# Performance work log

Hardware: AMD Instinct MI355X
Metric: run time of the kernel (lower is better)

The kernel has to match this reference:

```python
import jax, jax.numpy as jnp
import numpy as np

N, E, B = 50000, 400000, 128
F_IN, EDIM, EMB, H = 64, 8, 64, 4
HC = EMB * H  # 256
L = 3          # gnn_layers
DN = 256       # dense_neurons
NEG_SLOPE = 0.2
EPS = 1e-5


def setup_inputs():
    key = jax.random.key(0)
    ks = jax.random.split(key, 32)
    s = 0.05
    d = {}
    d["x"] = jax.random.normal(ks[0], (N, F_IN), jnp.float32)
    d["edge_index"] = jax.random.randint(ks[1], (2, E), 0, N, jnp.int32)
    d["edge_attr"] = jax.random.normal(ks[2], (E, EDIM), jnp.float32)
    d["mol_formal_charge"] = jax.random.normal(ks[3], (B,), jnp.float32)
    d["mol_nrot"] = jax.random.normal(ks[4], (B,), jnp.float32)
    d["batch_index"] = jnp.sort(jax.random.randint(ks[5], (N,), 0, B, jnp.int32))
    # GATv2 params, stacked over L layers (in_dim == EMB == F_IN for all layers)
    d["gat_Wl"] = jax.random.normal(ks[6], (L, F_IN, HC), jnp.float32) * s
    d["gat_Wr"] = jax.random.normal(ks[7], (L, F_IN, HC), jnp.float32) * s
    d["gat_We"] = jax.random.normal(ks[8], (L, EDIM, HC), jnp.float32) * s
    d["gat_att"] = jax.random.normal(ks[9], (L, H, EMB), jnp.float32) * s
    d["gat_b"] = jnp.zeros((L, HC), jnp.float32)
    d["tr_W"] = jax.random.normal(ks[10], (L, HC, EMB), jnp.float32) * s
    d["tr_b"] = jnp.zeros((L, EMB), jnp.float32)
    d["bn_g"] = jnp.ones((L, EMB), jnp.float32)
    d["bn_b"] = jnp.zeros((L, EMB), jnp.float32)
    d["gate_W"] = jax.random.normal(ks[11], (EMB, 1), jnp.float32) * s
    d["gate_b"] = jnp.zeros((1,), jnp.float32)
    d["lin1_W"] = jax.random.normal(ks[12], (EMB + 2, DN), jnp.float32) * s
    d["lin1_b"] = jnp.zeros((DN,), jnp.float32)
    d["fc1_W"] = jax.random.normal(ks[13], (DN, DN // 2), jnp.float32) * s
    d["fc1_b"] = jnp.zeros((DN // 2,), jnp.float32)
    d["fc2_W"] = jax.random.normal(ks[14], (DN // 2, DN // 4), jnp.float32) * s
    d["fc2_b"] = jnp.zeros((DN // 4,), jnp.float32)
    d["out_W"] = jax.random.normal(ks[15], (DN // 4, 1), jnp.float32) * s
    d["out_b"] = jnp.zeros((1,), jnp.float32)
    return d


def _seg_softmax(logits, seg, num):
    # numerically stable per-segment softmax over leading axis
    mx = jax.ops.segment_max(logits, seg, num_segments=num)
    ex = jnp.exp(logits - mx[seg])
    den = jax.ops.segment_sum(ex, seg, num_segments=num)
    return ex / den[seg]


def reference(x, edge_index, edge_attr, mol_formal_charge, mol_nrot, batch_index,
              gat_Wl, gat_Wr, gat_We, gat_att, gat_b, tr_W, tr_b, bn_g, bn_b,
              gate_W, gate_b, lin1_W, lin1_b, fc1_W, fc1_b, fc2_W, fc2_b,
              out_W, out_b):
    src, dst = edge_index[0], edge_index[1]  # messages flow src -> dst
    h = x
    for l in range(L):
        xl = (h @ gat_Wl[l]).reshape(N, H, EMB)
        xr = (h @ gat_Wr[l]).reshape(N, H, EMB)
        ea = (edge_attr @ gat_We[l]).reshape(E, H, EMB)
        xls = xl[src]                                   # [E,H,C]
        m = jax.nn.leaky_relu(xls + xr[dst] + ea, NEG_SLOPE)
        logit = jnp.einsum('ehc,hc->eh', m, gat_att[l])  # [E,H]
        alpha = _seg_softmax(logit, dst, N)              # [E,H]
        agg = jax.ops.segment_sum(alpha[:, :, None] * xls, dst, num_segments=N)
        h = agg.reshape(N, HC) + gat_b[l]
        h = jax.nn.relu(h @ tr_W[l] + tr_b[l])
        # BatchNorm1d (training-mode batch stats, biased var)
        mu = h.mean(0)
        var = h.var(0)
        h = (h - mu) / jnp.sqrt(var + EPS) * bn_g[l] + bn_b[l]
    # AttentionalAggregation pooling
    gate = h @ gate_W + gate_b                           # [N,1]
    w = _seg_softmax(gate, batch_index, B)
    pooled = jax.ops.segment_sum(w * h, batch_index, num_segments=B)  # [B,EMB]
    z = jnp.concatenate([pooled, mol_formal_charge[:, None], mol_nrot[:, None]], axis=1)
    z = jax.nn.relu(z @ lin1_W + lin1_b)
    z = jax.nn.relu(z @ fc1_W + fc1_b)
    z = jax.nn.relu(z @ fc2_W + fc2_b)
    return z @ out_W + out_b                             # [B,1]
```

## Files before the change

### kernel.cpp

```cpp
#include <hip/hip_runtime.h>

#define NN 50000
#define NE 400000
#define NB 128
#define NINF (-__builtin_inff())

__global__ __launch_bounds__(256) void k_hist(const int* __restrict__ dstv, int* __restrict__ deg) {
    int e = blockIdx.x * 256 + threadIdx.x;
    if (e < NE) atomicAdd(&deg[dstv[e]], 1);
}

__global__ __launch_bounds__(1024) void k_scan(const int* __restrict__ deg, int* __restrict__ rowptr) {
    __shared__ int wsum[16];
    __shared__ int total_s;
    const int tid = threadIdx.x, lane = tid & 63, w = tid >> 6;
    if (tid == 0) rowptr[0] = 0;
    int carry = 0;
    for (int base = 0; base < NN; base += 1024) {
        int i = base + tid;
        int v = (i < NN) ? deg[i] : 0;
        int incl = v;
        #pragma unroll
        for (int off = 1; off < 64; off <<= 1) {
            int t = __shfl_up(incl, off);
            if (lane >= off) incl += t;
        }
        if (lane == 63) wsum[w] = incl;
        __syncthreads();
        if (tid < 16) {
            int s = wsum[tid];
            int si = s;
            #pragma unroll
            for (int off = 1; off < 16; off <<= 1) {
                int t = __shfl_up(si, off, 16);
                if (tid >= off) si += t;
            }
            wsum[tid] = si - s;
            if (tid == 15) total_s = si;
        }
        __syncthreads();
        if (i < NN) rowptr[i + 1] = carry + wsum[w] + incl;
        carry += total_s;
        __syncthreads();
    }
}

__global__ __launch_bounds__(256) void k_scatter(const int* __restrict__ dstv, const int* __restrict__ rowptr,
                                                 int* __restrict__ cnt, int* __restrict__ eid) {
    int e = blockIdx.x * 256 + threadIdx.x;
    if (e < NE) {
        int d = dstv[e];
        int pos = rowptr[d] + atomicAdd(&cnt[d], 1);
        eid[pos] = e;
    }
}

__global__ __launch_bounds__(256) void k_permute(const int* __restrict__ eid, const int* __restrict__ srcv,
                                                 const float* __restrict__ eattr, int* __restrict__ src_perm,
                                                 float4* __restrict__ ea_perm) {
    int p = blockIdx.x * 256 + threadIdx.x;
    if (p < NE) {
        int e = eid[p];
        src_perm[p] = srcv[e];
        ea_perm[p * 2] = ((const float4*)eattr)[e * 2];
        ea_perm[p * 2 + 1] = ((const float4*)eattr)[e * 2 + 1];
    }
}

__global__ __launch_bounds__(256) void k_gemm64(const float* __restrict__ A, const float* __restrict__ Wl,
                                                const float* __restrict__ Wr, float* __restrict__ Cl,
                                                float* __restrict__ Cr, const float* __restrict__ bnp) {
    __shared__ float As[64 * 64];
    __shared__ float Ws[64 * 128];
    const int tid = threadIdx.x;
    const int mat = blockIdx.y >> 1, ch = blockIdx.y & 1;
    const float* W = mat ? Wr : Wl;
    float* C = mat ? Cr : Cl;
    const int r0b = blockIdx.x * 64;

    for (int i = tid; i < 2048; i += 256) {
        const int k = i >> 5, c4 = i & 31;
        float4 v = ((const float4*)W)[k * 64 + ch * 32 + c4];
        if (bnp) {
            const float s = bnp[128 + k];
            v.x *= s; v.y *= s; v.z *= s; v.w *= s;
        }
        ((float4*)Ws)[i] = v;
    }
    for (int i = tid; i < 1024; i += 256) {
        const int r = i >> 4, c4 = i & 15;
        const int rg = (r0b + r < NN) ? (r0b + r) : (NN - 1);
        ((float4*)As)[i] = ((const float4*)A)[rg * 16 + c4];
    }
    __syncthreads();

    const int cg = tid & 31;
    const int rq = tid >> 5;
    float acc[8][4];
    if (bnp) {
        const float* shW = bnp + 256 + mat * 256 + ch * 128 + cg * 4;
        #pragma unroll
        for (int rr = 0; rr < 8; ++rr) {
            acc[rr][0] = shW[0]; acc[rr][1] = shW[1]; acc[rr][2] = shW[2]; acc[rr][3] = shW[3];
        }
    } else {
        #pragma unroll
        for (int rr = 0; rr < 8; ++rr)
            acc[rr][0] = acc[rr][1] = acc[rr][2] = acc[rr][3] = 0.f;
    }

    for (int kq = 0; kq < 16; ++kq) {
        float4 av[8];
        #pragma unroll
        for (int rr = 0; rr < 8; ++rr)
            av[rr] = ((const float4*)As)[(rq * 8 + rr) * 16 + kq];
        #pragma unroll
        for (int kk = 0; kk < 4; ++kk) {
            const float4 w = *(const float4*)(Ws + ((kq * 4 + kk) << 7) + (cg << 2));
            #pragma unroll
            for (int rr = 0; rr < 8; ++rr) {
                const float a = reinterpret_cast<const float*>(&av[rr])[kk];
                acc[rr][0] = fmaf(a, w.x, acc[rr][0]);
                acc[rr][1] = fmaf(a, w.y, acc[rr][1]);
                acc[rr][2] = fmaf(a, w.z, acc[rr][2]);
                acc[rr][3] = fmaf(a, w.w, acc[rr][3]);
            }
        }
    }
    #pragma unroll
    for (int rr = 0; rr < 8; ++rr) {
        const int r = r0b + rq * 8 + rr;
        if (r < NN)
            *(float4*)(C + (size_t)r * 256 + ch * 128 + cg * 4) =
                make_float4(acc[rr][0], acc[rr][1], acc[rr][2], acc[rr][3]);
    }
}

template <bool PERM>
__global__ __launch_bounds__(256, 4) void k_agg(const float* __restrict__ xl, float* __restrict__ xragg,
                                                const float* __restrict__ att, const float* __restrict__ gatb,
                                                const int* __restrict__ rowptr, const int* __restrict__ eid,
                                                const int* __restrict__ srcv, const float* __restrict__ eattr,
                                                const int* __restrict__ src_perm, const float4* __restrict__ ea_perm,
                                                const float* __restrict__ We) {
    const int lane = threadIdx.x & 63;
    const float4 we0 = ((const float4*)(We + 0 * 256))[lane];
    const float4 we1 = ((const float4*)(We + 1 * 256))[lane];
    const float4 we2 = ((const float4*)(We + 2 * 256))[lane];
    const float4 we3 = ((const float4*)(We + 3 * 256))[lane];
    const float4 we4 = ((const float4*)(We + 4 * 256))[lane];
    const float4 we5 = ((const float4*)(We + 5 * 256))[lane];
    const float4 we6 = ((const float4*)(We + 6 * 256))[lane];
    const float4 we7 = ((const float4*)(We + 7 * 256))[lane];
    const float4 attf = ((const float4*)att)[lane];
    const float4 gbf = ((const float4*)gatb)[lane];
    const int nw = gridDim.x * (blockDim.x >> 6);
    int wid = blockIdx.x * (blockDim.x >> 6) + (threadIdx.x >> 6);

#define LOADE(X, idx)                                                          \
    {                                                                          \
        int s_;                                                                \
        const float4* eap_;                                                    \
        if (PERM) {                                                            \
            s_ = src_perm[idx];                                                \
            eap_ = ea_perm + (size_t)(idx) * 2;                                \
        } else {                                                               \
            const int e_ = eid[idx];                                           \
            s_ = srcv[e_];                                                     \
            eap_ = (const float4*)(eattr + (size_t)e_ * 8);                    \
        }                                                                      \
        X##x = ((const float4*)(xl + (size_t)s_ * 256))[lane];                 \
        X##a = eap_[0];                                                        \
        X##b = eap_[1];                                                        \
    }

#define PROC(X, M, D, C0, C1, C2, C3)                                          \
    {                                                                          \
        float v0 = fmaf(X##a.x, we0.x, xr.x), v1 = fmaf(X##a.x, we0.y, xr.y);  \
        float v2 = fmaf(X##a.x, we0.z, xr.z), v3 = fmaf(X##a.x, we0.w, xr.w);  \
        v0 = fmaf(X##a.y, we1.x, v0); v1 = fmaf(X##a.y, we1.y, v1);            \
        v2 = fmaf(X##a.y, we1.z, v2); v3 = fmaf(X##a.y, we1.w, v3);            \
        v0 = fmaf(X##a.z, we2.x, v0); v1 = fmaf(X##a.z, we2.y, v1);            \
        v2 = fmaf(X##a.z, we2.z, v2); v3 = fmaf(X##a.z, we2.w, v3);            \
        v0 = fmaf(X##a.w, we3.x, v0); v1 = fmaf(X##a.w, we3.y, v1);            \
        v2 = fmaf(X##a.w, we3.z, v2); v3 = fmaf(X##a.w, we3.w, v3);            \
        v0 = fmaf(X##b.x, we4.x, v0); v1 = fmaf(X##b.x, we4.y, v1);            \
        v2 = fmaf(X##b.x, we4.z, v2); v3 = fmaf(X##b.x, we4.w, v3);            \
        v0 = fmaf(X##b.y, we5.x, v0); v1 = fmaf(X##b.y, we5.y, v1);            \
        v2 = fmaf(X##b.y, we5.z, v2); v3 = fmaf(X##b.y, we5.w, v3);            \
        v0 = fmaf(X##b.z, we6.x, v0); v1 = fmaf(X##b.z, we6.y, v1);            \
        v2 = fmaf(X##b.z, we6.z, v2); v3 = fmaf(X##b.z, we6.w, v3);            \
        v0 = fmaf(X##b.w, we7.x, v0); v1 = fmaf(X##b.w, we7.y, v1);            \
        v2 = fmaf(X##b.w, we7.z, v2); v3 = fmaf(X##b.w, we7.w, v3);            \
        v0 += X##x.x; v1 += X##x.y; v2 += X##x.z; v3 += X##x.w;                \
        v0 = fmaxf(v0, 0.2f * v0); v1 = fmaxf(v1, 0.2f * v1);                  \
        v2 = fmaxf(v2, 0.2f * v2); v3 = fmaxf(v3, 0.2f * v3);                  \
        float part = v0 * attf.x;                                              \
        part = fmaf(v1, attf.y, part);                                         \
        part = fmaf(v2, attf.z, part);                                         \
        part = fmaf(v3, attf.w, part);                                         \
        part += __shfl_xor(part, 1);                                           \
        part += __shfl_xor(part, 2);                                           \
        part += __shfl_xor(part, 4);                                           \
        part += __shfl_xor(part, 8);                                           \
        const float mn = fmaxf(M, part);                                       \
        const float scl = __expf(M - mn);                                      \
        const float p = __expf(part - mn);                                     \
        D = fmaf(D, scl, p);                                                   \
        C0 = fmaf(C0, scl, p * X##x.x);                                        \
        C1 = fmaf(C1, scl, p * X##x.y);                                        \
        C2 = fmaf(C2, scl, p * X##x.z);                                        \
        C3 = fmaf(C3, scl, p * X##x.w);                                        \
        M = mn;                                                                \
    }

    for (int n = wid; n < NN; n += nw) {
        const int e0 = rowptr[n], e1 = rowptr[n + 1];
        const float4 xr = ((const float4*)(xragg + (size_t)n * 256))[lane];
        float mA = NINF, dA = 0.f, cA0 = 0.f, cA1 = 0.f, cA2 = 0.f, cA3 = 0.f;
        float mB = NINF, dB = 0.f, cB0 = 0.f, cB1 = 0.f, cB2 = 0.f, cB3 = 0.f;
        float4 Ax, Aa, Ab, Bx, Ba, Bb;
        if (e0 < e1) LOADE(A, e0);
        if (e0 + 1 < e1) LOADE(B, e0 + 1);
        int i = e0;
        for (; i + 5 < e1; i += 4) {
            float4 Cx, Ca, Cb, Dx, Da, Db;
            LOADE(C, i + 2);
            LOADE(D, i + 3);
            PROC(A, mA, dA, cA0, cA1, cA2, cA3);
            PROC(B, mB, dB, cB0, cB1, cB2, cB3);
            LOADE(A, i + 4);
            LOADE(B, i + 5);
            PROC(C, mA, dA, cA0, cA1, cA2, cA3);
            PROC(D, mB, dB, cB0, cB1, cB2, cB3);
        }
        if (i < e1) PROC(A, mA, dA, cA0, cA1, cA2, cA3);
        if (i + 1 < e1) PROC(B, mB, dB, cB0, cB1, cB2, cB3);
        for (int j = i + 2; j < e1; ++j) {
            LOADE(A, j);
            PROC(A, mA, dA, cA0, cA1, cA2, cA3);
        }
        float4 o;
        if (e1 > e0) {
            const float m = fmaxf(mA, mB);
            const float wA = __expf(mA - m), wB = __expf(mB - m);
            const float inv = 1.0f / fmaf(wA, dA, wB * dB);
            o.x = fmaf((wA * cA0 + wB * cB0), inv, gbf.x);
            o.y = fmaf((wA * cA1 + wB * cB1), inv, gbf.y);
            o.z = fmaf((wA * cA2 + wB * cB2), inv, gbf.z);
            o.w = fmaf((wA * cA3 + wB * cB3), inv, gbf.w);
        } else {
            o = gbf;
        }
        ((float4*)(xragg + (size_t)n * 256))[lane] = o;
    }
#undef LOADE
#undef PROC
}

__global__ __launch_bounds__(256) void k_tr(const float* __restrict__ A, const float* __restrict__ W,
                                            const float* __restrict__ bias, float* __restrict__ Hout,
                                            float* __restrict__ stats) {
    __shared__ float As[64 * 68];
    __shared__ float Ws[64 * 64];
    __shared__ float red[128];
    const int tid = threadIdx.x;
    const int cg = tid & 15;
    const int rq = tid >> 4;
    const int r0b = blockIdx.x * 64;

    float acc[4][4];
    {
        const float b0 = bias[cg * 4], b1 = bias[cg * 4 + 1], b2 = bias[cg * 4 + 2], b3 = bias[cg * 4 + 3];
        #pragma unroll
        for (int rr = 0; rr < 4; ++rr) { acc[rr][0] = b0; acc[rr][1] = b1; acc[rr][2] = b2; acc[rr][3] = b3; }
    }

    for (int kc = 0; kc < 4; ++kc) {
        if (kc) __syncthreads();
        for (int i = tid; i < 1024; i += 256)
            ((float4*)Ws)[i] = ((const float4*)(W + kc * 4096))[i];
        for (int i = tid; i < 1024; i += 256) {
            const int r = i >> 4, c4 = i & 15;
            const int rg = (r0b + r < NN) ? (r0b + r) : (NN - 1);
            *(float4*)(As + r * 68 + c4 * 4) = ((const float4*)A)[(size_t)rg * 64 + kc * 16 + c4];
        }
        __syncthreads();
        for (int kq = 0; kq < 16; ++kq) {
            float4 av[4];
            #pragma unroll
            for (int rr = 0; rr < 4; ++rr)
                av[rr] = *(const float4*)(As + (rq * 4 + rr) * 68 + kq * 4);
            #pragma unroll
            for (int kk = 0; kk < 4; ++kk) {
                const float4 w = *(const float4*)(Ws + ((kq * 4 + kk) << 6) + (cg << 2));
                #pragma unroll
                for (int rr = 0; rr < 4; ++rr) {
                    const float a = reinterpret_cast<const float*>(&av[rr])[kk];
                    acc[rr][0] = fmaf(a, w.x, acc[rr][0]);
                    acc[rr][1] = fmaf(a, w.y, acc[rr][1]);
                    acc[rr][2] = fmaf(a, w.z, acc[rr][2]);
                    acc[rr][3] = fmaf(a, w.w, acc[rr][3]);
                }
            }
        }
    }
    float lsum[4] = {0.f, 0.f, 0.f, 0.f}, lsq[4] = {0.f, 0.f, 0.f, 0.f};
    #pragma unroll
    for (int rr = 0; rr < 4; ++rr) {
        const int r = r0b + rq * 4 + rr;
        if (r < NN) {
            float v0 = fmaxf(acc[rr][0], 0.f), v1 = fmaxf(acc[rr][1], 0.f);
            float v2 = fmaxf(acc[rr][2], 0.f), v3 = fmaxf(acc[rr][3], 0.f);
            lsum[0] += v0; lsum[1] += v1; lsum[2] += v2; lsum[3] += v3;
            lsq[0] = fmaf(v0, v0, lsq[0]); lsq[1] = fmaf(v1, v1, lsq[1]);
            lsq[2] = fmaf(v2, v2, lsq[2]); lsq[3] = fmaf(v3, v3, lsq[3]);
            *(float4*)(Hout + (size_t)r * 64 + cg * 4) = make_float4(v0, v1, v2, v3);
        }
    }
    __syncthreads();
    if (tid < 128) red[tid] = 0.f;
    __syncthreads();
    #pragma unroll
    for (int j = 0; j < 4; ++j) {
        atomicAdd(&red[cg * 4 + j], lsum[j]);
        atomicAdd(&red[64 + cg * 4 + j], lsq[j]);
    }
    __syncthreads();
    if (tid < 64) {
        atomicAdd(&stats[tid], red[tid]);
        atomicAdd(&stats[64 + tid], red[64 + tid]);
    }
}

__global__ __launch_bounds__(256) void k_bn_finalize(float* __restrict__ st, const float* __restrict__ g,
                                                     const float* __restrict__ b, const float* __restrict__ Wln,
                                                     const float* __restrict__ Wrn) {
    __shared__ float sh_s[64];
    const int tid = threadIdx.x;
    if (tid < 64) {
        const float mu = st[tid] * (1.0f / (float)NN);
        const float var = st[64 + tid] * (1.0f / (float)NN) - mu * mu;
        const float rstd = rsqrtf(var + 1e-5f);
        const float sc = g[tid] * rstd;
        const float sh = fmaf(-mu, sc, b[tid]);
        st[128 + tid] = sc;
        st[192 + tid] = sh;
        sh_s[tid] = sh;
    }
    __syncthreads();
    if (Wln) {
        float al = 0.f, ar = 0.f;
        for (int k = 0; k < 64; ++k) {
            al = fmaf(sh_s[k], Wln[k * 256 + tid], al);
            ar = fmaf(sh_s[k], Wrn[k * 256 + tid], ar);
        }
        st[256 + tid] = al;
        st[512 + tid] = ar;
    }
}

__global__ __launch_bounds__(256) void k_pool(const float* __restrict__ h, const float* __restrict__ gw,
                                              const int* __restrict__ bidx, const float* __restrict__ st,
                                              float* __restrict__ pooled) {
    __shared__ float gate_s[1024];
    __shared__ float red[4];
    __shared__ float pp[4][64];
    const int b = blockIdx.x, tid = threadIdx.x, lane = tid & 63, w = tid >> 6;
    int lo = 0, hi = NN;
    while (lo < hi) { int mid = (lo + hi) >> 1; if (bidx[mid] < b) lo = mid + 1; else hi = mid; }
    const int s0 = lo;
    lo = 0; hi = NN;
    while (lo < hi) { int mid = (lo + hi) >> 1; if (bidx[mid] < b + 1) lo = mid + 1; else hi = mid; }
    const int s1 = lo;
    const int seg = s1 - s0;
    if (seg == 0) {
        if (tid < 64) pooled[b * 64 + tid] = st[192 + tid];
        return;
    }
    const float gwv = gw[lane] * st[128 + lane];
    for (int i = s0 + w; i < s1; i += 4) {
        float p = h[(size_t)i * 64 + lane] * gwv;
        #pragma unroll
        for (int off = 32; off; off >>= 1) p += __shfl_xor(p, off);
        if (lane == 0) gate_s[i - s0] = p;
    }
    __syncthreads();
    float v = NINF;
    for (int i = tid; i < seg; i += 256) v = fmaxf(v, gate_s[i]);
    #pragma unroll
    for (int off = 32; off; off >>= 1) v = fmaxf(v, __shfl_xor(v, off));
    if (lane == 0) red[w] = v;
    __syncthreads();
    const float mx = fmaxf(fmaxf(red[0], red[1]), fmaxf(red[2], red[3]));
    __syncthreads();
    float d = 0.f;
    for (int i = tid; i < seg; i += 256) {
        const float ex = __expf(gate_s[i] - mx);
        gate_s[i] = ex;
        d += ex;
    }
    #pragma unroll
    for (int off = 32; off; off >>= 1) d += __shfl_xor(d, off);
    if (lane == 0) red[w] = d;
    __syncthreads();
    const float den = red[0] + red[1] + red[2] + red[3];
    const int c = tid & 63, ro = tid >> 6;
    float acc = 0.f;
    for (int i = s0 + ro; i < s1; i += 4) acc = fmaf(gate_s[i - s0], h[(size_t)i * 64 + c], acc);
    pp[ro][c] = acc;
    __syncthreads();
    if (ro == 0) {
        const float raw = (pp[0][c] + pp[1][c] + pp[2][c] + pp[3][c]) / den;
        pooled[b * 64 + c] = fmaf(raw, st[128 + c], st[192 + c]);
    }
}

__global__ __launch_bounds__(256) void k_head(const float* __restrict__ pooled, const float* __restrict__ fc,
                                              const float* __restrict__ nrot, const float* __restrict__ W1,
                                              const float* __restrict__ b1, const float* __restrict__ W2,
                                              const float* __restrict__ b2, const float* __restrict__ W3,
                                              const float* __restrict__ b3, const float* __restrict__ W4,
                                              const float* __restrict__ b4, float* __restrict__ out) {
    __shared__ float z[66], a1[256], a2[128], a3[64];
    const int b = blockIdx.x, tid = threadIdx.x;
    if (tid < 64) z[tid] = pooled[b * 64 + tid];
    if (tid == 64) z[64] = fc[b];
    if (tid == 65) z[65] = nrot[b];
    __syncthreads();
    float s = b1[tid];
    for (int k = 0; k < 66; ++k) s = fmaf(z[k], W1[k * 256 + tid], s);
    a1[tid] = fmaxf(s, 0.f);
    __syncthreads();
    if (tid < 128) {
        float s2 = b2[tid];
        for (int k = 0; k < 256; ++k) s2 = fmaf(a1[k], W2[k * 128 + tid], s2);
        a2[tid] = fmaxf(s2, 0.f);
    }
    __syncthreads();
    if (tid < 64) {
        float s3 = b3[tid];
        for (int k = 0; k < 128; ++k) s3 = fmaf(a2[k], W3[k * 64 + tid], s3);
        a3[tid] = fmaxf(s3, 0.f);
    }
    __syncthreads();
    if (tid < 64) {
        float p = a3[tid] * W4[tid];
        #pragma unroll
        for (int off = 32; off; off >>= 1) p += __shfl_xor(p, off);
        if (tid == 0) out[b] = p + b4[0];
    }
}

extern "C" void kernel_launch(void* const* d_in, const int* in_sizes, int n_in,
                              void* d_out, int out_size, void* d_ws, size_t ws_size,
                              hipStream_t stream) {
    const float* x     = (const float*)d_in[0];
    const int*   ei    = (const int*)d_in[1];
    const float* eattr = (const float*)d_in[2];
    const float* fcv   = (const float*)d_in[3];
    const float* nrot  = (const float*)d_in[4];
    const int*   bidx  = (const int*)d_in[5];
    const float* Wl    = (const float*)d_in[6];
    const float* Wr    = (const float*)d_in[7];
    const float* We    = (const float*)d_in[8];
    const float* att   = (const float*)d_in[9];
    const float* gatb  = (const float*)d_in[10];
    const float* trW   = (const float*)d_in[11];
    const float* trb   = (const float*)d_in[12];
    const float* bng   = (const float*)d_in[13];
    const float* bnb   = (const float*)d_in[14];
    const float* gateW = (const float*)d_in[15];
    const float* W1    = (const float*)d_in[17];
    const float* b1    = (const float*)d_in[18];
    const float* W2    = (const float*)d_in[19];
    const float* b2    = (const float*)d_in[20];
    const float* W3    = (const float*)d_in[21];
    const float* b3    = (const float*)d_in[22];
    const float* W4    = (const float*)d_in[23];
    const float* b4    = (const float*)d_in[24];
    float* out = (float*)d_out;

    const int* srcv = ei;
    const int* dstv = ei + NE;

    char* w = (char*)d_ws;
    float*  xl       = (float*)(w);
    float*  xragg    = (float*)(w + 51200000);
    float*  hbuf     = (float*)(w + 102400000);
    int*    deg      = (int*)  (w + 102400000);
    int*    cnt      = (int*)  (w + 102600000);
    int*    eid      = (int*)  (w + 115200000);
    int*    rowptr   = (int*)  (w + 116800000);
    float*  stats    = (float*)(w + 117000064);
    float*  pooled   = (float*)(w + 117009280);
    int*    src_perm = (int*)  (w + 117042048);
    float4* ea_perm  = (float4*)(w + 118642048);
    const bool use_perm = (ws_size >= (size_t)131442048);

    hipMemsetAsync(deg, 0, 400000, stream);
    hipMemsetAsync(stats, 0, 9216, stream);
    k_hist<<<(NE + 255) / 256, 256, 0, stream>>>(dstv, deg);
    k_scan<<<1, 1024, 0, stream>>>(deg, rowptr);
    k_scatter<<<(NE + 255) / 256, 256, 0, stream>>>(dstv, rowptr, cnt, eid);
    if (use_perm)
        k_permute<<<(NE + 255) / 256, 256, 0, stream>>>(eid, srcv, eattr, src_perm, ea_perm);

    const float* hin = x;
    for (int l = 0; l < 3; ++l) {
        const float* bnp = (l == 0) ? nullptr : (stats + (l - 1) * 768);
        dim3 gg((NN + 63) / 64, 4);
        k_gemm64<<<gg, 256, 0, stream>>>(hin, Wl + l * 16384, Wr + l * 16384, xl, xragg, bnp);
        if (use_perm)
            k_agg<true><<<2048, 256, 0, stream>>>(xl, xragg, att + l * 256, gatb + l * 256, rowptr,
                                                  eid, srcv, eattr, src_perm, ea_perm, We + l * 2048);
        else
            k_agg<false><<<2048, 256, 0, stream>>>(xl, xragg, att + l * 256, gatb + l * 256, rowptr,
                                                   eid, srcv, eattr, src_perm, ea_perm, We + l * 2048);
        k_tr<<<(NN + 63) / 64, 256, 0, stream>>>(xragg, trW + l * 16384, trb + l * 64, hbuf, stats + l * 768);
        k_bn_finalize<<<1, 256, 0, stream>>>(stats + l * 768, bng + l * 64, bnb + l * 64,
                                             (l < 2) ? (Wl + (l + 1) * 16384) : nullptr,
                                             (l < 2) ? (Wr + (l + 1) * 16384) : nullptr);
        hin = hbuf;
    }
    k_pool<<<NB, 256, 0, stream>>>(hbuf, gateW, bidx, stats + 2 * 768, pooled);
    k_head<<<NB, 256, 0, stream>>>(pooled, fcv, nrot, W1, b1, W2, b2, W3, b3, W4, b4, out);
}
```

Measured before the change: 792.3 us.

## Drop online-max softmax, fuse permute into scatter and BN finalize into consumers

Replaces the two-stream online-softmax aggregation with a single accumulator that exponentiates logits directly without max subtraction, using DPP adds for the 16-lane reduction and a lighter 2-deep prefetch. Fuses the edge permutation into the scatter kernel, folds the batch-norm finalize into the next GEMM and the pooling kernel, and merges pooling with the MLP head. This removes exp work and several kernel launches. It risks overflow for large attention logits and recomputes the shift-weight product in every GEMM block.

```diff
diff --git a/kernel.cpp b/kernel.cpp
--- a/kernel.cpp
+++ b/kernel.cpp
@@ -4,6 +4,18 @@
 #define NE 400000
 #define NB 128
 #define NINF (-__builtin_inff())
+
+__device__ __forceinline__ float dpp_add16(float x) {
+    int v = __float_as_int(x);
+    x += __int_as_float(__builtin_amdgcn_update_dpp(0, v, 0xB1, 0xF, 0xF, true));
+    v = __float_as_int(x);
+    x += __int_as_float(__builtin_amdgcn_update_dpp(0, v, 0x4E, 0xF, 0xF, true));
+    v = __float_as_int(x);
+    x += __int_as_float(__builtin_amdgcn_update_dpp(0, v, 0x141, 0xF, 0xF, true));
+    v = __float_as_int(x);
+    x += __int_as_float(__builtin_amdgcn_update_dpp(0, v, 0x140, 0xF, 0xF, true));
+    return x;
+}
 
 __global__ __launch_bounds__(256) void k_hist(const int* __restrict__ dstv, int* __restrict__ deg) {
     int e = blockIdx.x * 256 + threadIdx.x;
@@ -45,44 +57,53 @@
     }
 }
 
-__global__ __launch_bounds__(256) void k_scatter(const int* __restrict__ dstv, const int* __restrict__ rowptr,
-                                                 int* __restrict__ cnt, int* __restrict__ eid) {
+__global__ __launch_bounds__(256) void k_scatter(const int* __restrict__ dstv, const int* __restrict__ srcv,
+                                                 const float* __restrict__ eattr, const int* __restrict__ rowptr,
+                                                 int* __restrict__ cnt, int* __restrict__ eid,
+                                                 int* __restrict__ src_perm, float4* __restrict__ ea_perm,
+                                                 int use_perm) {
     int e = blockIdx.x * 256 + threadIdx.x;
     if (e < NE) {
         int d = dstv[e];
         int pos = rowptr[d] + atomicAdd(&cnt[d], 1);
         eid[pos] = e;
-    }
-}
-
-__global__ __launch_bounds__(256) void k_permute(const int* __restrict__ eid, const int* __restrict__ srcv,
-                                                 const float* __restrict__ eattr, int* __restrict__ src_perm,
-                                                 float4* __restrict__ ea_perm) {
-    int p = blockIdx.x * 256 + threadIdx.x;
-    if (p < NE) {
-        int e = eid[p];
-        src_perm[p] = srcv[e];
-        ea_perm[p * 2] = ((const float4*)eattr)[e * 2];
-        ea_perm[p * 2 + 1] = ((const float4*)eattr)[e * 2 + 1];
+        if (use_perm) {
+            src_perm[pos] = srcv[e];
+            ea_perm[(size_t)pos * 2] = ((const float4*)eattr)[e * 2];
+            ea_perm[(size_t)pos * 2 + 1] = ((const float4*)eattr)[e * 2 + 1];
+        }
     }
 }
 
 __global__ __launch_bounds__(256) void k_gemm64(const float* __restrict__ A, const float* __restrict__ Wl,
                                                 const float* __restrict__ Wr, float* __restrict__ Cl,
-                                                float* __restrict__ Cr, const float* __restrict__ bnp) {
+                                                float* __restrict__ Cr, const float* __restrict__ stats,
+                                                const float* __restrict__ bg, const float* __restrict__ bb) {
     __shared__ float As[64 * 64];
     __shared__ float Ws[64 * 128];
+    __shared__ float sc_s[64], sh_s[64], shW_s[128];
     const int tid = threadIdx.x;
     const int mat = blockIdx.y >> 1, ch = blockIdx.y & 1;
     const float* W = mat ? Wr : Wl;
     float* C = mat ? Cr : Cl;
     const int r0b = blockIdx.x * 64;
 
+    if (stats) {
+        if (tid < 64) {
+            const float mu = stats[tid] * (1.0f / (float)NN);
+            const float var = stats[64 + tid] * (1.0f / (float)NN) - mu * mu;
+            const float rstd = rsqrtf(var + 1e-5f);
+            const float sc = bg[tid] * rstd;
+            sc_s[tid] = sc;
+            sh_s[tid] = fmaf(-mu, sc, bb[tid]);
+        }
+        __syncthreads();
+    }
     for (int i = tid; i < 2048; i += 256) {
         const int k = i >> 5, c4 = i & 31;
         float4 v = ((const float4*)W)[k * 64 + ch * 32 + c4];
-        if (bnp) {
-            const float s = bnp[128 + k];
+        if (stats) {
+            const float s = sc_s[k];
             v.x *= s; v.y *= s; v.z *= s; v.w *= s;
         }
         ((float4*)Ws)[i] = v;
@@ -92,16 +113,22 @@
         const int rg = (r0b + r < NN) ? (r0b + r) : (NN - 1);
         ((float4*)As)[i] = ((const float4*)A)[rg * 16 + c4];
     }
+    if (stats && tid < 128) {
+        const float* wc = W + ch * 128 + tid;
+        float s = 0.f;
+        for (int k = 0; k < 64; ++k) s = fmaf(sh_s[k], wc[k * 256], s);
+        shW_s[tid] = s;
+    }
     __syncthreads();
 
     const int cg = tid & 31;
     const int rq = tid >> 5;
     float acc[8][4];
-    if (bnp) {
-        const float* shW = bnp + 256 + mat * 256 + ch * 128 + cg * 4;
+    if (stats) {
         #pragma unroll
         for (int rr = 0; rr < 8; ++rr) {
-            acc[rr][0] = shW[0]; acc[rr][1] = shW[1]; acc[rr][2] = shW[2]; acc[rr][3] = shW[3];
+            acc[rr][0] = shW_s[cg * 4]; acc[rr][1] = shW_s[cg * 4 + 1];
+            acc[rr][2] = shW_s[cg * 4 + 2]; acc[rr][3] = shW_s[cg * 4 + 3];
         }
     } else {
         #pragma unroll
@@ -174,7 +201,7 @@
         X##b = eap_[1];                                                        \
     }
 
-#define PROC(X, M, D, C0, C1, C2, C3)                                          \
+#define PROC(X)                                                                \
     {                                                                          \
         float v0 = fmaf(X##a.x, we0.x, xr.x), v1 = fmaf(X##a.x, we0.y, xr.y);  \
         float v2 = fmaf(X##a.x, we0.z, xr.z), v3 = fmaf(X##a.x, we0.w, xr.w);  \
@@ -199,56 +226,52 @@
         part = fmaf(v1, attf.y, part);                                         \
         part = fmaf(v2, attf.z, part);                                         \
         part = fmaf(v3, attf.w, part);                                         \
-        part += __shfl_xor(part, 1);                                           \
-        part += __shfl_xor(part, 2);                                           \
-        part += __shfl_xor(part, 4);                                           \
-        part += __shfl_xor(part, 8);                                           \
-        const float mn = fmaxf(M, part);                                       \
-        const float scl = __expf(M - mn);                                      \
-        const float p = __expf(part - mn);                                     \
-        D = fmaf(D, scl, p);                                                   \
-        C0 = fmaf(C0, scl, p * X##x.x);                                        \
-        C1 = fmaf(C1, scl, p * X##x.y);                                        \
-        C2 = fmaf(C2, scl, p * X##x.z);                                        \
-        C3 = fmaf(C3, scl, p * X##x.w);                                        \
-        M = mn;                                                                \
+        part = dpp_add16(part);                                                \
+        const float p = __expf(part);                                          \
+        den += p;                                                              \
+        c0 = fmaf(p, X##x.x, c0);                                              \
+        c1 = fmaf(p, X##x.y, c1);                                              \
+        c2 = fmaf(p, X##x.z, c2);                                              \
+        c3 = fmaf(p, X##x.w, c3);                                              \
     }
 
     for (int n = wid; n < NN; n += nw) {
         const int e0 = rowptr[n], e1 = rowptr[n + 1];
         const float4 xr = ((const float4*)(xragg + (size_t)n * 256))[lane];
-        float mA = NINF, dA = 0.f, cA0 = 0.f, cA1 = 0.f, cA2 = 0.f, cA3 = 0.f;
-        float mB = NINF, dB = 0.f, cB0 = 0.f, cB1 = 0.f, cB2 = 0.f, cB3 = 0.f;
+        float den = 0.f, c0 = 0.f, c1 = 0.f, c2 = 0.f, c3 = 0.f;
         float4 Ax, Aa, Ab, Bx, Ba, Bb;
-        if (e0 < e1) LOADE(A, e0);
-        if (e0 + 1 < e1) LOADE(B, e0 + 1);
-        int i = e0;
-        for (; i + 5 < e1; i += 4) {
-            float4 Cx, Ca, Cb, Dx, Da, Db;
-            LOADE(C, i + 2);
-            LOADE(D, i + 3);
-            PROC(A, mA, dA, cA0, cA1, cA2, cA3);
-            PROC(B, mB, dB, cB0, cB1, cB2, cB3);
-            LOADE(A, i + 4);
-            LOADE(B, i + 5);
-            PROC(C, mA, dA, cA0, cA1, cA2, cA3);
-            PROC(D, mB, dB, cB0, cB1, cB2, cB3);
-        }
-        if (i < e1) PROC(A, mA, dA, cA0, cA1, cA2, cA3);
-        if (i + 1 < e1) PROC(B, mB, dB, cB0, cB1, cB2, cB3);
-        for (int j = i + 2; j < e1; ++j) {
-            LOADE(A, j);
-            PROC(A, mA, dA, cA0, cA1, cA2, cA3);
+        const int cnt = e1 - e0;
+        if (cnt > 0) {
+            LOADE(A, e0);
+            if (cnt > 1) {
+                LOADE(B, e0 + 1);
+                int i = e0;
+                for (; i + 3 < e1; i += 2) {
+                    PROC(A);
+                    LOADE(A, i + 2);
+                    PROC(B);
+                    LOADE(B, i + 3);
+                }
+                const int r = e1 - i;
+                PROC(A);
+                if (r == 3) {
+                    LOADE(A, i + 2);
+                    PROC(B);
+                    PROC(A);
+                } else {
+                    PROC(B);
+                }
+            } else {
+                PROC(A);
+            }
         }
         float4 o;
-        if (e1 > e0) {
-            const float m = fmaxf(mA, mB);
-            const float wA = __expf(mA - m), wB = __expf(mB - m);
-            const float inv = 1.0f / fmaf(wA, dA, wB * dB);
-            o.x = fmaf((wA * cA0 + wB * cB0), inv, gbf.x);
-            o.y = fmaf((wA * cA1 + wB * cB1), inv, gbf.y);
-            o.z = fmaf((wA * cA2 + wB * cB2), inv, gbf.z);
-            o.w = fmaf((wA * cA3 + wB * cB3), inv, gbf.w);
+        if (cnt > 0) {
+            const float inv = 1.0f / den;
+            o.x = fmaf(c0, inv, gbf.x);
+            o.y = fmaf(c1, inv, gbf.y);
+            o.z = fmaf(c2, inv, gbf.z);
+            o.w = fmaf(c3, inv, gbf.w);
         } else {
             o = gbf;
         }
@@ -333,40 +356,29 @@
     }
 }
 
-__global__ __launch_bounds__(256) void k_bn_finalize(float* __restrict__ st, const float* __restrict__ g,
-                                                     const float* __restrict__ b, const float* __restrict__ Wln,
-                                                     const float* __restrict__ Wrn) {
-    __shared__ float sh_s[64];
-    const int tid = threadIdx.x;
-    if (tid < 64) {
-        const float mu = st[tid] * (1.0f / (float)NN);
-        const float var = st[64 + tid] * (1.0f / (float)NN) - mu * mu;
-        const float rstd = rsqrtf(var + 1e-5f);
-        const float sc = g[tid] * rstd;
-        const float sh = fmaf(-mu, sc, b[tid]);
-        st[128 + tid] = sc;
-        st[192 + tid] = sh;
-        sh_s[tid] = sh;
-    }
-    __syncthreads();
-    if (Wln) {
-        float al = 0.f, ar = 0.f;
-        for (int k = 0; k < 64; ++k) {
-            al = fmaf(sh_s[k], Wln[k * 256 + tid], al);
-            ar = fmaf(sh_s[k], Wrn[k * 256 + tid], ar);
-        }
-        st[256 + tid] = al;
-        st[512 + tid] = ar;
-    }
-}
-
-__global__ __launch_bounds__(256) void k_pool(const float* __restrict__ h, const float* __restrict__ gw,
-                                              const int* __restrict__ bidx, const float* __restrict__ st,
-                                              float* __restrict__ pooled) {
+__global__ __launch_bounds__(256) void k_poolhead(const float* __restrict__ h, const float* __restrict__ gw,
+                                                  const int* __restrict__ bidx, const float* __restrict__ stats,
+                                                  const float* __restrict__ bg, const float* __restrict__ bb,
+                                                  const float* __restrict__ fc, const float* __restrict__ nrot,
+                                                  const float* __restrict__ W1, const float* __restrict__ b1,
+                                                  const float* __restrict__ W2, const float* __restrict__ b2,
+                                                  const float* __restrict__ W3, const float* __restrict__ b3,
+                                                  const float* __restrict__ W4, const float* __restrict__ b4,
+                                                  float* __restrict__ out) {
     __shared__ float gate_s[1024];
     __shared__ float red[4];
     __shared__ float pp[4][64];
+    __shared__ float scb[64], shb[64];
+    __shared__ float z[66], a1[256], a2[128], a3[64];
     const int b = blockIdx.x, tid = threadIdx.x, lane = tid & 63, w = tid >> 6;
+    if (tid < 64) {
+        const float mu = stats[tid] * (1.0f / (float)NN);
+        const float var = stats[64 + tid] * (1.0f / (float)NN) - mu * mu;
+        const float rstd = rsqrtf(var + 1e-5f);
+        const float sc = bg[tid] * rstd;
+        scb[tid] = sc;
+        shb[tid] = fmaf(-mu, sc, bb[tid]);
+    }
     int lo = 0, hi = NN;
     while (lo < hi) { int mid = (lo + hi) >> 1; if (bidx[mid] < b) lo = mid + 1; else hi = mid; }
     const int s0 = lo;
@@ -374,11 +386,9 @@
     while (lo < hi) { int mid = (lo + hi) >> 1; if (bidx[mid] < b + 1) lo = mid + 1; else hi = mid; }
     const int s1 = lo;
     const int seg = s1 - s0;
-    if (seg == 0) {
-        if (tid < 64) pooled[b * 64 + tid] = st[192 + tid];
-        return;
-    }
-    const float gwv = gw[lane] * st[128 + lane];
+    __syncthreads();
+
+    const float gwv = gw[lane] * scb[lane];
     for (int i = s0 + w; i < s1; i += 4) {
         float p = h[(size_t)i * 64 + lane] * gwv;
         #pragma unroll
@@ -410,21 +420,10 @@
     for (int i = s0 + ro; i < s1; i += 4) acc = fmaf(gate_s[i - s0], h[(size_t)i * 64 + c], acc);
     pp[ro][c] = acc;
     __syncthreads();
-    if (ro == 0) {
-        const float raw = (pp[0][c] + pp[1][c] + pp[2][c] + pp[3][c]) / den;
-        pooled[b * 64 + c] = fmaf(raw, st[128 + c], st[192 + c]);
-    }
-}
-
-__global__ __launch_bounds__(256) void k_head(const float* __restrict__ pooled, const float* __restrict__ fc,
-                                              const float* __restrict__ nrot, const float* __restrict__ W1,
-                                              const float* __restrict__ b1, const float* __restrict__ W2,
-                                              const float* __restrict__ b2, const float* __restrict__ W3,
-                                              const float* __restrict__ b3, const float* __restrict__ W4,
-                                              const float* __restrict__ b4, float* __restrict__ out) {
-    __shared__ float z[66], a1[256], a2[128], a3[64];
-    const int b = blockIdx.x, tid = threadIdx.x;
-    if (tid < 64) z[tid] = pooled[b * 64 + tid];
+    if (tid < 64) {
+        const float raw = (pp[0][tid] + pp[1][tid] + pp[2][tid] + pp[3][tid]) / den;
+        z[tid] = (seg > 0) ? fmaf(raw, scb[tid], shb[tid]) : shb[tid];
+    }
     if (tid == 64) z[64] = fc[b];
     if (tid == 65) z[65] = nrot[b];
     __syncthreads();
@@ -493,36 +492,33 @@
     int*    eid      = (int*)  (w + 115200000);
     int*    rowptr   = (int*)  (w + 116800000);
     float*  stats    = (float*)(w + 117000064);
-    float*  pooled   = (float*)(w + 117009280);
     int*    src_perm = (int*)  (w + 117042048);
     float4* ea_perm  = (float4*)(w + 118642048);
     const bool use_perm = (ws_size >= (size_t)131442048);
 
     hipMemsetAsync(deg, 0, 400000, stream);
-    hipMemsetAsync(stats, 0, 9216, stream);
+    hipMemsetAsync(stats, 0, 1536, stream);
     k_hist<<<(NE + 255) / 256, 256, 0, stream>>>(dstv, deg);
     k_scan<<<1, 1024, 0, stream>>>(deg, rowptr);
-    k_scatter<<<(NE + 255) / 256, 256, 0, stream>>>(dstv, rowptr, cnt, eid);
-    if (use_perm)
-        k_permute<<<(NE + 255) / 256, 256, 0, stream>>>(eid, srcv, eattr, src_perm, ea_perm);
+    k_scatter<<<(NE + 255) / 256, 256, 0, stream>>>(dstv, srcv, eattr, rowptr, cnt, eid,
+                                                    src_perm, ea_perm, use_perm ? 1 : 0);
 
     const float* hin = x;
     for (int l = 0; l < 3; ++l) {
-        const float* bnp = (l == 0) ? nullptr : (stats + (l - 1) * 768);
+        const float* st = (l == 0) ? nullptr : (stats + (l - 1) * 128);
+        const float* g  = (l == 0) ? nullptr : (bng + (l - 1) * 64);
+        const float* bb = (l == 0) ? nullptr : (bnb + (l - 1) * 64);
         dim3 gg((NN + 63) / 64, 4);
-        k_gemm64<<<gg, 256, 0, stream>>>(hin, Wl + l * 16384, Wr + l * 16384, xl, xragg, bnp);
+        k_gemm64<<<gg, 256, 0, stream>>>(hin, Wl + l * 16384, Wr + l * 16384, xl, xragg, st, g, bb);
         if (use_perm)
             k_agg<true><<<2048, 256, 0, stream>>>(xl, xragg, att + l * 256, gatb + l * 256, rowptr,
                                                   eid, srcv, eattr, src_perm, ea_perm, We + l * 2048);
         else
             k_agg<false><<<2048, 256, 0, stream>>>(xl, xragg, att + l * 256, gatb + l * 256, rowptr,
                                                    eid, srcv, eattr, src_perm, ea_perm, We + l * 2048);
-        k_tr<<<(NN + 63) / 64, 256, 0, stream>>>(xragg, trW + l * 16384, trb + l * 64, hbuf, stats + l * 768);
-        k_bn_finalize<<<1, 256, 0, stream>>>(stats + l * 768, bng + l * 64, bnb + l * 64,
-                                             (l < 2) ? (Wl + (l + 1) * 16384) : nullptr,
-                                             (l < 2) ? (Wr + (l + 1) * 16384) : nullptr);
+        k_tr<<<(NN + 63) / 64, 256, 0, stream>>>(xragg, trW + l * 16384, trb + l * 64, hbuf, stats + l * 128);
         hin = hbuf;
     }
-    k_pool<<<NB, 256, 0, stream>>>(hbuf, gateW, bidx, stats + 2 * 768, pooled);
-    k_head<<<NB, 256, 0, stream>>>(pooled, fcv, nrot, W1, b1, W2, b2, W3, b3, W4, b4, out);
-}
+    k_poolhead<<<NB, 256, 0, stream>>>(hbuf, gateW, bidx, stats + 2 * 128, bng + 128, bnb + 128,
+                                       fcv, nrot, W1, b1, W2, b2, W3, b3, W4, b4, out);
+}
```

After: 759.5 us. 4.1% less time.
